# Performance work log

Measured on AMD Instinct MI355X. Metric: run time of the kernel, lower is better.

## Reference

```python
import jax, jax.numpy as jnp
import numpy as np

B, N, D_IN = 4, 2048, 1024
H, D_OUT = 8, 128


def setup_inputs() -> dict:
    key = jax.random.key(0)
    k1, k2, k3 = jax.random.split(key, 3)
    x = jax.random.normal(k1, (B, N, D_IN), dtype=jnp.float32)
    # W: (num_head, 3 [q,k,v], d_in, output_dim), glorot-ish scale
    W = jax.random.normal(k2, (H, 3, D_IN, D_OUT), dtype=jnp.float32) * (1.0 / np.sqrt(D_IN))
    Wo = jax.random.normal(k3, (H * D_OUT, D_OUT), dtype=jnp.float32) * (1.0 / np.sqrt(H * D_OUT))
    return {"x": x, "W": W, "Wo": Wo}


def reference(x, W, Wo):
    # Per-head QKV projections, vectorized over heads.
    # q,k,v: [B, H, N, D_OUT]
    q = jnp.einsum("bnd,hde->bhne", x, W[:, 0])
    k = jnp.einsum("bnd,hde->bhne", x, W[:, 1])
    v = jnp.einsum("bnd,hde->bhne", x, W[:, 2])
    scale = 1.0 / jnp.sqrt(jnp.asarray(D_OUT, dtype=x.dtype))
    # scores: [B, H, N, N]
    e = jnp.einsum("bhne,bhme->bhnm", q, k) * scale
    a = jax.nn.softmax(e, axis=-1)
    o = jnp.einsum("bhnm,bhme->bhne", a, v)  # [B, H, N, D_OUT]
    # concat heads -> [B, N, H*D_OUT]; head i occupies slice [i*D_OUT:(i+1)*D_OUT]
    o = jnp.transpose(o, (0, 2, 1, 3)).reshape(x.shape[0], x.shape[1], H * D_OUT)
    z = jnp.einsum("bnf,fe->bne", o, Wo)  # [B, N, D_OUT]
    return z
```

## Files before the change

### kernel.cpp

```cpp
#include <hip/hip_runtime.h>
#include <cstdint>


#define DEV __device__ __forceinline__

typedef _Float16 h8 __attribute__((ext_vector_type(8)));
typedef _Float16 h4 __attribute__((ext_vector_type(4)));
typedef _Float16 h2 __attribute__((ext_vector_type(2)));
typedef float f4 __attribute__((ext_vector_type(4)));
typedef float f16x16 __attribute__((ext_vector_type(16)));
typedef uint32_t u32x4 __attribute__((ext_vector_type(4)));
typedef uint32_t u32x2 __attribute__((ext_vector_type(2)));

typedef __attribute__((address_space(1))) const uint32_t gu32;
typedef __attribute__((address_space(3))) uint32_t lu32;

DEV float fexp2(float x) { return __builtin_amdgcn_exp2f(x); }

DEV f4 mfma16(h8 a, h8 b, f4 c) {
  return __builtin_amdgcn_mfma_f32_16x16x32_f16(a, b, c, 0, 0, 0);
}

DEV f16x16 mfma32(h8 a, h8 b, f16x16 c) {
  return __builtin_amdgcn_mfma_f32_32x32x16_f16(a, b, c, 0, 0, 0);
}

DEV void g2l16(void* lds, const void* g) {
  __builtin_amdgcn_global_load_lds((gu32*)(uintptr_t)g, (lu32*)(uintptr_t)lds,
                                   16, 0, 0);
}

DEV uint32_t pkrn(float a, float b) {
  h2 t;
  t[0] = (_Float16)a;
  t[1] = (_Float16)b;
  return __builtin_bit_cast(uint32_t, t);
}

DEV u32x2 pl32swap(uint32_t x, uint32_t y) {
  return __builtin_amdgcn_permlane32_swap(x, y, false, false);
}

__global__ __launch_bounds__(256) void cvt_all_kernel(
    const float* __restrict__ x, _Float16* __restrict__ Xb,
    const float* __restrict__ W, const float* __restrict__ Wo,
    _Float16* __restrict__ WT, _Float16* __restrict__ WoT) {
  __shared__ float st[64][68];
  const int bid = blockIdx.x;
  const int tid = threadIdx.x;
  if (bid < 8192) {
    size_t i = (size_t)(bid * 256 + tid) * 4;
    f4 v = *(const f4*)(x + i);
    h4 o;
    o[0] = (_Float16)v[0];
    o[1] = (_Float16)v[1];
    o[2] = (_Float16)v[2];
    o[3] = (_Float16)v[3];
    *(h4*)(Xb + i) = o;
    return;
  }
  const int idx0 = bid - 8192;
  const int mz = idx0 >> 5;
  const int rem = idx0 & 31;
  const int d0 = (rem & 15) * 64;
  const int e0 = (rem >> 4) * 64;
  const float* src = (mz < 24) ? (W + (size_t)mz * 131072) : Wo;
  _Float16* dst = (mz < 24) ? (WT + (size_t)mz * 131072) : WoT;
#pragma unroll
  for (int r = 0; r < 4; ++r) {
    int idx = r * 256 + tid;
    int dd = idx >> 4, cc = (idx & 15) * 4;
    f4 v = *(const f4*)(src + (size_t)(d0 + dd) * 128 + e0 + cc);
    *(f4*)&st[dd][cc] = v;
  }
  __syncthreads();
#pragma unroll
  for (int r = 0; r < 2; ++r) {
    int idx = r * 256 + tid;
    int ee = idx >> 3, dd = (idx & 7) * 8;
    h8 o;
#pragma unroll
    for (int i = 0; i < 8; ++i) o[i] = (_Float16)st[dd + i][ee];
    *(h8*)(dst + (size_t)(e0 + ee) * 1024 + d0 + dd) = o;
  }
}

__global__ __launch_bounds__(256, 3) void gemm_qkv_kernel(
    const _Float16* __restrict__ A, const _Float16* __restrict__ BTall,
    _Float16* __restrict__ Qb, _Float16* __restrict__ Kb,
    _Float16* __restrict__ VTb) {
  constexpr int K = 1024;
  __shared__ __align__(16) _Float16 sAB[16384];
  const int tid = threadIdx.x;
  const int wave = tid >> 6, lane = tid & 63;
  const int g = lane >> 4, l15 = lane & 15;
  const int sw = l15 & 7;
  const int m0 = blockIdx.x * 128;
  const int j = blockIdx.y;
  const _Float16* BT = BTall + (size_t)j * (128 * 1024);

  f4 acc[4][4] = {};
  const int ar = (wave >> 1) * 64 + l15;
  const int br = (wave & 1) * 64 + l15;

#pragma unroll 1
  for (int kt = 0; kt < K; kt += 64) {
    __syncthreads();
#pragma unroll
    for (int r = 0; r < 4; ++r) {
      int idx = r * 256 + tid;
      int row = idx >> 3;
      int jg = (idx & 7) ^ (row & 7);
      g2l16(&sAB[idx * 8], A + (size_t)(m0 + row) * K + kt + jg * 8);
      g2l16(&sAB[8192 + idx * 8], BT + (size_t)row * K + kt + jg * 8);
    }
    __syncthreads();
#pragma unroll
    for (int ks = 0; ks < 2; ++ks) {
      int off = ((ks * 4 + g) ^ sw) * 8;
      h8 af[4], bf[4];
#pragma unroll
      for (int mt = 0; mt < 4; ++mt)
        af[mt] = *(const h8*)&sAB[(ar + mt * 16) * 64 + off];
#pragma unroll
      for (int nt = 0; nt < 4; ++nt)
        bf[nt] = *(const h8*)&sAB[8192 + (br + nt * 16) * 64 + off];
#pragma unroll
      for (int mt = 0; mt < 4; ++mt)
#pragma unroll
        for (int nt = 0; nt < 4; ++nt)
          acc[mt][nt] = mfma16(af[mt], bf[nt], acc[mt][nt]);
    }
  }

  const int wr = (wave >> 1) * 64, wc = (wave & 1) * 64;
  const int h = j / 3, s = j - h * 3;
  if (s < 2) {
    const float scl = (s == 0) ? 0.12751741032075984f : 1.0f;
    _Float16* dst = (s == 0) ? Qb : Kb;
    __syncthreads();
#pragma unroll
    for (int mt = 0; mt < 4; ++mt)
#pragma unroll
      for (int rg = 0; rg < 4; ++rg) {
        int rl = wr + mt * 16 + g * 4 + rg;
#pragma unroll
        for (int nt = 0; nt < 4; ++nt) {
          int c = wc + nt * 16 + l15;
          sAB[rl * 128 + (((c >> 3) ^ (rl & 7)) * 8) + (c & 7)] =
              (_Float16)(acc[mt][nt][rg] * scl);
        }
      }
    __syncthreads();
    int rr = tid >> 1, seg = tid & 1;
    int m = m0 + rr, b = m >> 11, n = m & 2047;
    size_t rb = ((size_t)((b * 8 + h) * 2048 + n)) * 128;
#pragma unroll
    for (int k = 0; k < 8; ++k) {
      int ch = seg * 8 + k;
      h8 v = *(const h8*)&sAB[rr * 128 + ((ch ^ (rr & 7)) * 8)];
      *(h8*)&dst[rb + ch * 8] = v;
    }
  } else {
    __syncthreads();
    const int b = m0 >> 11, n0 = m0 & 2047;
    size_t base = (size_t)(b * 8 + h) * (128 * 2048);
#pragma unroll
    for (int mt = 0; mt < 4; ++mt)
#pragma unroll
      for (int rg = 0; rg < 4; ++rg) {
        int nl = wr + mt * 16 + g * 4 + rg;
        int cc = (nl >> 3), ci = nl & 7;
#pragma unroll
        for (int nt = 0; nt < 4; ++nt) {
          int c = wc + nt * 16 + l15;
          sAB[c * 128 + ((cc ^ (c & 7)) * 8) + ci] = (_Float16)acc[mt][nt][rg];
        }
      }
    __syncthreads();
    int c = tid >> 1, seg = tid & 1;
#pragma unroll
    for (int k = 0; k < 8; ++k) {
      int ch = seg * 8 + k;
      h8 v = *(const h8*)&sAB[c * 128 + ((ch ^ (c & 7)) * 8)];
      *(h8*)&VTb[base + (size_t)c * 2048 + n0 + ch * 8] = v;
    }
  }
}

__global__ __launch_bounds__(256, 2) void flash_kernel(
    const _Float16* __restrict__ Qb, const _Float16* __restrict__ Kb,
    const _Float16* __restrict__ VTb, _Float16* __restrict__ Oc) {
  __shared__ __align__(16) _Float16 sK[2][64 * 128];
  __shared__ __align__(16) _Float16 sVT[2][128 * 64];
  const int tid = threadIdx.x, wave = tid >> 6, lane = tid & 63;
  const int l31 = lane & 31, hi = lane >> 5;
  const int sw = l31 & 7;
  const int bh = blockIdx.x, b = bh >> 3, h = bh & 7;
  const int q0 = blockIdx.y * 128;
  const _Float16* Q = Qb + (size_t)bh * (2048 * 128);
  const _Float16* Kp = Kb + (size_t)bh * (2048 * 128);
  const _Float16* VT = VTb + (size_t)bh * (128 * 2048);

  h8 qf[8];
#pragma unroll
  for (int c = 0; c < 8; ++c)
    qf[c] = *(const h8*)&Q[(size_t)(q0 + wave * 32 + l31) * 128 + c * 16 +
                           hi * 8];

  f16x16 oacc[4] = {};
  float lsum = 0.0f;

#define STAGE(buf, kv0)                                                        \
  {                                                                            \
    _Float16* dK = &sK[buf][0];                                                \
    _Float16* dV = &sVT[buf][0];                                               \
    _Pragma("unroll") for (int i = 0; i < 4; ++i) {                            \
      int idx = i * 256 + tid;                                                 \
      int rk = idx >> 4, ck = idx & 15;                                        \
      g2l16(dK + idx * 8,                                                      \
            Kp + (size_t)((kv0) + rk) * 128 + ((ck ^ (rk & 7)) * 8));          \
      int rv = idx >> 3, cv = idx & 7;                                         \
      g2l16(dV + idx * 8,                                                      \
            VT + (size_t)rv * 2048 + (kv0) + ((cv ^ (rv & 7)) * 8));           \
    }                                                                          \
  }

  STAGE(0, 0);
  int cur = 0;
#pragma unroll 1
  for (int t = 0; t < 32; ++t) {
    __syncthreads();
    if (t < 31) STAGE(cur ^ 1, (t + 1) * 64);
    const _Float16* bK = &sK[cur][0];
    const _Float16* bV = &sVT[cur][0];

    f16x16 s0 = {}, s1 = {};
#pragma unroll
    for (int c = 0; c < 8; ++c) {
      int off = ((c * 2 + hi) ^ sw) * 8;
      h8 a0 = *(const h8*)&bK[l31 * 128 + off];
      h8 a1 = *(const h8*)&bK[(32 + l31) * 128 + off];
      s0 = mfma32(a0, qf[c], s0);
      s1 = mfma32(a1, qf[c], s1);
    }

    uint32_t w0[8], w1[8];
#pragma unroll
    for (int j = 0; j < 8; ++j) {
      float a0 = fexp2(s0[2 * j]), b0 = fexp2(s0[2 * j + 1]);
      float a1 = fexp2(s1[2 * j]), b1 = fexp2(s1[2 * j + 1]);
      lsum += (a0 + b0) + (a1 + b1);
      w0[j] = pkrn(a0, b0);
      w1[j] = pkrn(a1, b1);
    }

    h8 pf[4];
#pragma unroll
    for (int half = 0; half < 2; ++half) {
      u32x2 r0 = pl32swap(w0[half * 4 + 0], w0[half * 4 + 2]);
      u32x2 r1 = pl32swap(w0[half * 4 + 1], w0[half * 4 + 3]);
      u32x4 tt;
      tt[0] = r0[0];
      tt[1] = r1[0];
      tt[2] = r0[1];
      tt[3] = r1[1];
      pf[half] = __builtin_bit_cast(h8, tt);
      u32x2 r2 = pl32swap(w1[half * 4 + 0], w1[half * 4 + 2]);
      u32x2 r3 = pl32swap(w1[half * 4 + 1], w1[half * 4 + 3]);
      u32x4 uu;
      uu[0] = r2[0];
      uu[1] = r3[0];
      uu[2] = r2[1];
      uu[3] = r3[1];
      pf[2 + half] = __builtin_bit_cast(h8, uu);
    }

#pragma unroll
    for (int dt = 0; dt < 4; ++dt) {
#pragma unroll
      for (int c = 0; c < 4; ++c) {
        int off = ((c * 2 + hi) ^ sw) * 8;
        h8 vf = *(const h8*)&bV[(dt * 32 + l31) * 64 + off];
        oacc[dt] = mfma32(vf, pf[c], oacc[dt]);
      }
    }
    cur ^= 1;
  }
#undef STAGE

  lsum += __shfl_xor(lsum, 32, 64);
  const float inv = 1.0f / lsum;

  __syncthreads();
  _Float16* sO = &sK[0][0] + wave * 4096;
#pragma unroll
  for (int dt = 0; dt < 4; ++dt)
#pragma unroll
    for (int r = 0; r < 16; ++r) {
      int d = dt * 32 + (r & 3) + 8 * (r >> 2) + 4 * hi;
      sO[l31 * 128 + (d ^ (sw << 3))] = (_Float16)(oacc[dt][r] * inv);
    }
  const int l15 = lane & 15, gq = lane >> 4;
#pragma unroll
  for (int it = 0; it < 8; ++it) {
    int q = it * 4 + gq;
    h8 v = *(const h8*)&sO[q * 128 + ((l15 ^ (q & 7)) * 8)];
    int n = q0 + wave * 32 + q;
    *(h8*)&Oc[((size_t)(b * 2048 + n)) * 1024 + h * 128 + l15 * 8] = v;
  }
}

__global__ __launch_bounds__(256, 4) void gemm_out_kernel(
    const _Float16* __restrict__ A, const _Float16* __restrict__ BT,
    float* __restrict__ outF) {
  __shared__ __align__(16) _Float16 sA[16 * 64];
  __shared__ __align__(16) _Float16 sB[128 * 64];
  const int tid = threadIdx.x, wave = tid >> 6, lane = tid & 63;
  const int g = lane >> 4, l15 = lane & 15, sw = l15 & 7;
  const int m0 = blockIdx.x * 16;
  f4 acc[2] = {};

#pragma unroll 1
  for (int kt = 0; kt < 1024; kt += 64) {
    __syncthreads();
    if (tid < 128) {
      int row = tid >> 3;
      int jg = (tid & 7) ^ (row & 7);
      g2l16(&sA[tid * 8], A + (size_t)(m0 + row) * 1024 + kt + jg * 8);
    }
#pragma unroll
    for (int r = 0; r < 4; ++r) {
      int idx = r * 256 + tid;
      int row = idx >> 3;
      int jg = (idx & 7) ^ (row & 7);
      g2l16(&sB[idx * 8], BT + (size_t)row * 1024 + kt + jg * 8);
    }
    __syncthreads();
#pragma unroll
    for (int ks = 0; ks < 2; ++ks) {
      int off = ((ks * 4 + g) ^ sw) * 8;
      h8 af = *(const h8*)&sA[l15 * 64 + off];
#pragma unroll
      for (int nt = 0; nt < 2; ++nt) {
        h8 bf = *(const h8*)&sB[(wave * 32 + nt * 16 + l15) * 64 + off];
        acc[nt] = mfma16(af, bf, acc[nt]);
      }
    }
  }
#pragma unroll
  for (int rg = 0; rg < 4; ++rg) {
    int m = m0 + g * 4 + rg;
#pragma unroll
    for (int nt = 0; nt < 2; ++nt)
      outF[(size_t)m * 128 + wave * 32 + nt * 16 + l15] = acc[nt][rg];
  }
}

extern "C" void kernel_launch(void* const* d_in, const int* in_sizes, int n_in,
                              void* d_out, int out_size, void* d_ws,
                              size_t ws_size, hipStream_t stream) {
  const float* x = (const float*)d_in[0];
  const float* W = (const float*)d_in[1];
  const float* Wo = (const float*)d_in[2];
  float* out = (float*)d_out;
  char* ws = (char*)d_ws;

  _Float16* Xb = (_Float16*)(ws + 0);
  _Float16* WT = (_Float16*)(ws + 16777216);
  _Float16* WoT = (_Float16*)(ws + 23068672);
  _Float16* Qb = (_Float16*)(ws + 23330816);
  _Float16* Kb = (_Float16*)(ws + 40108032);
  _Float16* VTb = (_Float16*)(ws + 56885248);
  _Float16* Oc = (_Float16*)(ws + 73662464);

  cvt_all_kernel<<<8992, 256, 0, stream>>>(x, Xb, W, Wo, WT, WoT);
  gemm_qkv_kernel<<<dim3(64, 24), 256, 0, stream>>>(Xb, WT, Qb, Kb, VTb);
  flash_kernel<<<dim3(32, 16), 256, 0, stream>>>(Qb, Kb, VTb, Oc);
  gemm_out_kernel<<<512, 256, 0, stream>>>(Oc, WoT, out);
}
```

Baseline: 241.5 us.

## Enlarge QKV GEMM tile to 256x128 using 32x32x16 MFMA

The QKV projection GEMM now computes a 256x128 output tile per block instead of 128x128. Each wave owns a 128x64 sub-tile built from 32x32x16 MFMA instructions rather than 16x16x32. The aim is higher arithmetic intensity per LDS load and fewer B-tile reloads, at the cost of a larger shared buffer, more accumulator registers, and half as many blocks. The epilogue is split into two halves so the 256-row tile can be staged through the existing shared memory.

```diff
diff --git a/kernel.cpp b/kernel.cpp
--- a/kernel.cpp
+++ b/kernel.cpp
@@ -89,101 +89,116 @@
     const _Float16* __restrict__ A, const _Float16* __restrict__ BTall,
     _Float16* __restrict__ Qb, _Float16* __restrict__ Kb,
     _Float16* __restrict__ VTb) {
-  constexpr int K = 1024;
-  __shared__ __align__(16) _Float16 sAB[16384];
+  __shared__ __align__(16) _Float16 sAB[24576];
   const int tid = threadIdx.x;
   const int wave = tid >> 6, lane = tid & 63;
-  const int g = lane >> 4, l15 = lane & 15;
-  const int sw = l15 & 7;
-  const int m0 = blockIdx.x * 128;
+  const int l31 = lane & 31, hi = lane >> 5;
+  const int sw = l31 & 7;
+  const int m0 = blockIdx.x * 256;
   const int j = blockIdx.y;
   const _Float16* BT = BTall + (size_t)j * (128 * 1024);
 
-  f4 acc[4][4] = {};
-  const int ar = (wave >> 1) * 64 + l15;
-  const int br = (wave & 1) * 64 + l15;
-
-#pragma unroll 1
-  for (int kt = 0; kt < K; kt += 64) {
-    __syncthreads();
+  const int wr = (wave >> 1) * 128;
+  const int wc = (wave & 1) * 64;
+
+  f16x16 acc[4][2] = {};
+
+#pragma unroll 1
+  for (int kt = 0; kt < 1024; kt += 64) {
+    __syncthreads();
+#pragma unroll
+    for (int r = 0; r < 8; ++r) {
+      int idx = r * 256 + tid;
+      int row = idx >> 3;
+      int jg = (idx & 7) ^ (row & 7);
+      g2l16(&sAB[idx * 8], A + (size_t)(m0 + row) * 1024 + kt + jg * 8);
+    }
 #pragma unroll
     for (int r = 0; r < 4; ++r) {
       int idx = r * 256 + tid;
       int row = idx >> 3;
       int jg = (idx & 7) ^ (row & 7);
-      g2l16(&sAB[idx * 8], A + (size_t)(m0 + row) * K + kt + jg * 8);
-      g2l16(&sAB[8192 + idx * 8], BT + (size_t)row * K + kt + jg * 8);
-    }
-    __syncthreads();
-#pragma unroll
-    for (int ks = 0; ks < 2; ++ks) {
-      int off = ((ks * 4 + g) ^ sw) * 8;
-      h8 af[4], bf[4];
-#pragma unroll
-      for (int mt = 0; mt < 4; ++mt)
-        af[mt] = *(const h8*)&sAB[(ar + mt * 16) * 64 + off];
-#pragma unroll
-      for (int nt = 0; nt < 4; ++nt)
-        bf[nt] = *(const h8*)&sAB[8192 + (br + nt * 16) * 64 + off];
-#pragma unroll
-      for (int mt = 0; mt < 4; ++mt)
-#pragma unroll
-        for (int nt = 0; nt < 4; ++nt)
-          acc[mt][nt] = mfma16(af[mt], bf[nt], acc[mt][nt]);
-    }
-  }
-
-  const int wr = (wave >> 1) * 64, wc = (wave & 1) * 64;
+      g2l16(&sAB[16384 + idx * 8], BT + (size_t)row * 1024 + kt + jg * 8);
+    }
+    __syncthreads();
+#pragma unroll
+    for (int s = 0; s < 4; ++s) {
+      int off = ((s * 2 + hi) ^ sw) * 8;
+      h8 bf[2];
+#pragma unroll
+      for (int ni = 0; ni < 2; ++ni)
+        bf[ni] = *(const h8*)&sAB[16384 + (wc + ni * 32 + l31) * 64 + off];
+#pragma unroll
+      for (int mi = 0; mi < 4; ++mi) {
+        h8 af = *(const h8*)&sAB[(wr + mi * 32 + l31) * 64 + off];
+#pragma unroll
+        for (int ni = 0; ni < 2; ++ni)
+          acc[mi][ni] = mfma32(af, bf[ni], acc[mi][ni]);
+      }
+    }
+  }
+
   const int h = j / 3, s = j - h * 3;
+  const int b = m0 >> 11, n0 = m0 & 2047;
   if (s < 2) {
     const float scl = (s == 0) ? 0.12751741032075984f : 1.0f;
     _Float16* dst = (s == 0) ? Qb : Kb;
-    __syncthreads();
-#pragma unroll
-    for (int mt = 0; mt < 4; ++mt)
-#pragma unroll
-      for (int rg = 0; rg < 4; ++rg) {
-        int rl = wr + mt * 16 + g * 4 + rg;
-#pragma unroll
-        for (int nt = 0; nt < 4; ++nt) {
-          int c = wc + nt * 16 + l15;
-          sAB[rl * 128 + (((c >> 3) ^ (rl & 7)) * 8) + (c & 7)] =
-              (_Float16)(acc[mt][nt][rg] * scl);
-        }
-      }
-    __syncthreads();
-    int rr = tid >> 1, seg = tid & 1;
-    int m = m0 + rr, b = m >> 11, n = m & 2047;
-    size_t rb = ((size_t)((b * 8 + h) * 2048 + n)) * 128;
-#pragma unroll
-    for (int k = 0; k < 8; ++k) {
-      int ch = seg * 8 + k;
-      h8 v = *(const h8*)&sAB[rr * 128 + ((ch ^ (rr & 7)) * 8)];
-      *(h8*)&dst[rb + ch * 8] = v;
+    size_t rbase = ((size_t)((b * 8 + h) * 2048 + n0)) * 128;
+#pragma unroll 1
+    for (int half = 0; half < 2; ++half) {
+      __syncthreads();
+      if ((wave >> 1) == half) {
+#pragma unroll
+        for (int mi = 0; mi < 4; ++mi)
+#pragma unroll
+          for (int reg = 0; reg < 16; ++reg) {
+            int rl = mi * 32 + (reg & 3) + 8 * (reg >> 2) + 4 * hi;
+#pragma unroll
+            for (int ni = 0; ni < 2; ++ni) {
+              int c = wc + ni * 32 + l31;
+              sAB[rl * 128 + (((c >> 3) ^ (rl & 7)) * 8) + (c & 7)] =
+                  (_Float16)(acc[mi][ni][reg] * scl);
+            }
+          }
+      }
+      __syncthreads();
+      int rr = tid >> 1, seg = tid & 1;
+      size_t rb = rbase + (size_t)(half * 128 + rr) * 128;
+#pragma unroll
+      for (int k = 0; k < 8; ++k) {
+        int ch = seg * 8 + k;
+        h8 v = *(const h8*)&sAB[rr * 128 + ((ch ^ (rr & 7)) * 8)];
+        *(h8*)&dst[rb + ch * 8] = v;
+      }
     }
   } else {
-    __syncthreads();
-    const int b = m0 >> 11, n0 = m0 & 2047;
     size_t base = (size_t)(b * 8 + h) * (128 * 2048);
-#pragma unroll
-    for (int mt = 0; mt < 4; ++mt)
-#pragma unroll
-      for (int rg = 0; rg < 4; ++rg) {
-        int nl = wr + mt * 16 + g * 4 + rg;
-        int cc = (nl >> 3), ci = nl & 7;
-#pragma unroll
-        for (int nt = 0; nt < 4; ++nt) {
-          int c = wc + nt * 16 + l15;
-          sAB[c * 128 + ((cc ^ (c & 7)) * 8) + ci] = (_Float16)acc[mt][nt][rg];
-        }
-      }
-    __syncthreads();
-    int c = tid >> 1, seg = tid & 1;
-#pragma unroll
-    for (int k = 0; k < 8; ++k) {
-      int ch = seg * 8 + k;
-      h8 v = *(const h8*)&sAB[c * 128 + ((ch ^ (c & 7)) * 8)];
-      *(h8*)&VTb[base + (size_t)c * 2048 + n0 + ch * 8] = v;
+#pragma unroll 1
+    for (int half = 0; half < 2; ++half) {
+      __syncthreads();
+      if ((wave >> 1) == half) {
+#pragma unroll
+        for (int mi = 0; mi < 4; ++mi)
+#pragma unroll
+          for (int reg = 0; reg < 16; ++reg) {
+            int nl = mi * 32 + (reg & 3) + 8 * (reg >> 2) + 4 * hi;
+            int cc = nl >> 3, ci = nl & 7;
+#pragma unroll
+            for (int ni = 0; ni < 2; ++ni) {
+              int c = wc + ni * 32 + l31;
+              sAB[c * 128 + ((cc ^ (c & 7)) * 8) + ci] =
+                  (_Float16)acc[mi][ni][reg];
+            }
+          }
+      }
+      __syncthreads();
+      int c = tid >> 1, seg = tid & 1;
+#pragma unroll
+      for (int k = 0; k < 8; ++k) {
+        int ch = seg * 8 + k;
+        h8 v = *(const h8*)&sAB[c * 128 + ((ch ^ (c & 7)) * 8)];
+        *(h8*)&VTb[base + (size_t)c * 2048 + n0 + half * 128 + ch * 8] = v;
+      }
     }
   }
 }
@@ -375,7 +390,7 @@
   _Float16* Oc = (_Float16*)(ws + 73662464);
 
   cvt_all_kernel<<<8992, 256, 0, stream>>>(x, Xb, W, Wo, WT, WoT);
-  gemm_qkv_kernel<<<dim3(64, 24), 256, 0, stream>>>(Xb, WT, Qb, Kb, VTb);
+  gemm_qkv_kernel<<<dim3(32, 24), 256, 0, stream>>>(Xb, WT, Qb, Kb, VTb);
   flash_kernel<<<dim3(32, 16), 256, 0, stream>>>(Qb, Kb, VTb, Oc);
   gemm_out_kernel<<<512, 256, 0, stream>>>(Oc, WoT, out);
 }
```

New measurement: 293.5 us. 21.5% more time.

## Double-buffer LDS tiles in QKV and output projection GEMMs

Applied to the files above, without the earlier changes.

Both GEMM kernels now keep two LDS stage buffers. Each iteration issues global-to-LDS loads for the next K tile before computing on the current one, which needs only one barrier per iteration instead of two. The output GEMM also doubles its K tile to 128, halving the loop count. The cost is twice the LDS footprint, so the launch bounds drop to 2 blocks per CU for both kernels, which may hurt latency hiding that previously came from occupancy.

```diff
diff --git a/kernel.cpp b/kernel.cpp
--- a/kernel.cpp
+++ b/kernel.cpp
@@ -85,12 +85,11 @@
   }
 }
 
-__global__ __launch_bounds__(256, 3) void gemm_qkv_kernel(
+__global__ __launch_bounds__(256, 2) void gemm_qkv_kernel(
     const _Float16* __restrict__ A, const _Float16* __restrict__ BTall,
     _Float16* __restrict__ Qb, _Float16* __restrict__ Kb,
     _Float16* __restrict__ VTb) {
-  constexpr int K = 1024;
-  __shared__ __align__(16) _Float16 sAB[16384];
+  __shared__ __align__(16) _Float16 sAB[2][16384];
   const int tid = threadIdx.x;
   const int wave = tid >> 6, lane = tid & 63;
   const int g = lane >> 4, l15 = lane & 15;
@@ -103,36 +102,48 @@
   const int ar = (wave >> 1) * 64 + l15;
   const int br = (wave & 1) * 64 + l15;
 
+#define QSTAGE(buf, kt)                                                        \
+  {                                                                            \
+    _Float16* dA = &sAB[buf][0];                                               \
+    _Float16* dB = &sAB[buf][8192];                                            \
+    _Pragma("unroll") for (int i = 0; i < 4; ++i) {                            \
+      int idx = i * 256 + tid;                                                 \
+      int row = idx >> 3;                                                      \
+      int jg = (idx & 7) ^ (row & 7);   \
+      g2l16(dA + idx * 8, A + (size_t)(m0 + row) * 1024 + (kt) + jg * 8);      \
+      g2l16(dB + idx * 8, BT + (size_t)row * 1024 + (kt) + jg * 8);            \
+    }                                                                          \
+  }
+
+  QSTAGE(0, 0);
+  int cur = 0;
 #pragma unroll 1
-  for (int kt = 0; kt < K; kt += 64) {
-    __syncthreads();
-#pragma unroll
-    for (int r = 0; r < 4; ++r) {
-      int idx = r * 256 + tid;
-      int row = idx >> 3;
-      int jg = (idx & 7) ^ (row & 7);
-      g2l16(&sAB[idx * 8], A + (size_t)(m0 + row) * K + kt + jg * 8);
-      g2l16(&sAB[8192 + idx * 8], BT + (size_t)row * K + kt + jg * 8);
-    }
-    __syncthreads();
+  for (int t = 0; t < 16; ++t) {
+    __syncthreads();
+    if (t < 15) QSTAGE(cur ^ 1, (t + 1) * 64);
+    const _Float16* bA = &sAB[cur][0];
+    const _Float16* bB = &sAB[cur][8192];
 #pragma unroll
     for (int ks = 0; ks < 2; ++ks) {
       int off = ((ks * 4 + g) ^ sw) * 8;
       h8 af[4], bf[4];
 #pragma unroll
       for (int mt = 0; mt < 4; ++mt)
-        af[mt] = *(const h8*)&sAB[(ar + mt * 16) * 64 + off];
+        af[mt] = *(const h8*)&bA[(ar + mt * 16) * 64 + off];
 #pragma unroll
       for (int nt = 0; nt < 4; ++nt)
-        bf[nt] = *(const h8*)&sAB[8192 + (br + nt * 16) * 64 + off];
+        bf[nt] = *(const h8*)&bB[(br + nt * 16) * 64 + off];
 #pragma unroll
       for (int mt = 0; mt < 4; ++mt)
 #pragma unroll
         for (int nt = 0; nt < 4; ++nt)
           acc[mt][nt] = mfma16(af[mt], bf[nt], acc[mt][nt]);
     }
-  }
-
+    cur ^= 1;
+  }
+#undef QSTAGE
+
+  _Float16* sE = &sAB[0][0];
   const int wr = (wave >> 1) * 64, wc = (wave & 1) * 64;
   const int h = j / 3, s = j - h * 3;
   if (s < 2) {
@@ -147,7 +158,7 @@
 #pragma unroll
         for (int nt = 0; nt < 4; ++nt) {
           int c = wc + nt * 16 + l15;
-          sAB[rl * 128 + (((c >> 3) ^ (rl & 7)) * 8) + (c & 7)] =
+          sE[rl * 128 + (((c >> 3) ^ (rl & 7)) * 8) + (c & 7)] =
               (_Float16)(acc[mt][nt][rg] * scl);
         }
       }
@@ -158,7 +169,7 @@
 #pragma unroll
     for (int k = 0; k < 8; ++k) {
       int ch = seg * 8 + k;
-      h8 v = *(const h8*)&sAB[rr * 128 + ((ch ^ (rr & 7)) * 8)];
+      h8 v = *(const h8*)&sE[rr * 128 + ((ch ^ (rr & 7)) * 8)];
       *(h8*)&dst[rb + ch * 8] = v;
     }
   } else {
@@ -174,7 +185,7 @@
 #pragma unroll
         for (int nt = 0; nt < 4; ++nt) {
           int c = wc + nt * 16 + l15;
-          sAB[c * 128 + ((cc ^ (c & 7)) * 8) + ci] = (_Float16)acc[mt][nt][rg];
+          sE[c * 128 + ((cc ^ (c & 7)) * 8) + ci] = (_Float16)acc[mt][nt][rg];
         }
       }
     __syncthreads();
@@ -182,7 +193,7 @@
 #pragma unroll
     for (int k = 0; k < 8; ++k) {
       int ch = seg * 8 + k;
-      h8 v = *(const h8*)&sAB[c * 128 + ((ch ^ (c & 7)) * 8)];
+      h8 v = *(const h8*)&sE[c * 128 + ((ch ^ (c & 7)) * 8)];
       *(h8*)&VTb[base + (size_t)c * 2048 + n0 + ch * 8] = v;
     }
   }
@@ -311,43 +322,48 @@
   }
 }
 
-__global__ __launch_bounds__(256, 4) void gemm_out_kernel(
+__global__ __launch_bounds__(256, 2) void gemm_out_kernel(
     const _Float16* __restrict__ A, const _Float16* __restrict__ BT,
     float* __restrict__ outF) {
-  __shared__ __align__(16) _Float16 sA[16 * 64];
-  __shared__ __align__(16) _Float16 sB[128 * 64];
+  __shared__ __align__(16) _Float16 sA[2][16 * 128];
+  __shared__ __align__(16) _Float16 sB[2][128 * 128];
   const int tid = threadIdx.x, wave = tid >> 6, lane = tid & 63;
   const int g = lane >> 4, l15 = lane & 15, sw = l15 & 7;
   const int m0 = blockIdx.x * 16;
   f4 acc[2] = {};
 
+#define OSTAGE(buf, kt)                                                        \
+  {                                                                            \
+    int rowa = tid >> 4, cka = tid & 15;                                       \
+    int jga = cka ^ (rowa & 7);                                                \
+    g2l16(&sA[buf][tid * 8], A + (size_t)(m0 + rowa) * 1024 + (kt) + jga * 8); \
+    _Pragma("unroll") for (int i = 0; i < 8; ++i) {                            \
+      int idx = i * 256 + tid;                                                 \
+      int row = idx >> 4, ck = idx & 15;                                       \
+      int jg = ck ^ (row & 7);                                                 \
+      g2l16(&sB[buf][idx * 8], BT + (size_t)row * 1024 + (kt) + jg * 8);       \
+    }                                                                          \
+  }
+
+  OSTAGE(0, 0);
+  int cur = 0;
 #pragma unroll 1
-  for (int kt = 0; kt < 1024; kt += 64) {
-    __syncthreads();
-    if (tid < 128) {
-      int row = tid >> 3;
-      int jg = (tid & 7) ^ (row & 7);
-      g2l16(&sA[tid * 8], A + (size_t)(m0 + row) * 1024 + kt + jg * 8);
-    }
-#pragma unroll
-    for (int r = 0; r < 4; ++r) {
-      int idx = r * 256 + tid;
-      int row = idx >> 3;
-      int jg = (idx & 7) ^ (row & 7);
-      g2l16(&sB[idx * 8], BT + (size_t)row * 1024 + kt + jg * 8);
-    }
-    __syncthreads();
-#pragma unroll
-    for (int ks = 0; ks < 2; ++ks) {
+  for (int t = 0; t < 8; ++t) {
+    __syncthreads();
+    if (t < 7) OSTAGE(cur ^ 1, (t + 1) * 128);
+#pragma unroll
+    for (int ks = 0; ks < 4; ++ks) {
       int off = ((ks * 4 + g) ^ sw) * 8;
-      h8 af = *(const h8*)&sA[l15 * 64 + off];
+      h8 af = *(const h8*)&sA[cur][l15 * 128 + off];
 #pragma unroll
       for (int nt = 0; nt < 2; ++nt) {
-        h8 bf = *(const h8*)&sB[(wave * 32 + nt * 16 + l15) * 64 + off];
+        h8 bf = *(const h8*)&sB[cur][(wave * 32 + nt * 16 + l15) * 128 + off];
         acc[nt] = mfma16(af, bf, acc[nt]);
       }
     }
-  }
+    cur ^= 1;
+  }
+#undef OSTAGE
 #pragma unroll
   for (int rg = 0; rg < 4; ++rg) {
     int m = m0 + g * 4 + rg;
```

Result: faster. 228.3 us (-5.4%).
